# Kernel optimization log

Measured on AMD Instinct MI355X. Metric: run time of the kernel, lower is better.

## Reference

```python
import jax, jax.numpy as jnp
import numpy as np

MARGIN = 0.2  # contrastive margin
# sim_type_dot = 'MISA': max over image regions, mean over (valid) words


def setup_inputs() -> dict:
    key = jax.random.key(0)
    k1, k2, k3, k4 = jax.random.split(key, 4)
    B, R, W, D = 128, 36, 60, 1024
    im = jax.random.normal(k1, (B, R, D), dtype=jnp.float32)
    s = jax.random.normal(k2, (B, W, D), dtype=jnp.float32)
    x = jax.random.normal(k3, (B, W, D), dtype=jnp.float32)  # unused in math, kept for API fidelity
    s_l = jax.random.randint(k4, (B,), 1, W + 1)  # caption lengths in [1, W]
    return {"im": im, "s": s, "s_l": s_l, "x": x}


def _scores(im, s, s_l):
    # im: (B, R, D) images; s: (B, W, D) captions; s_l: (B,) lengths
    B, W = s.shape[0], s.shape[1]
    # matchmap M[i, j, r, w] = <image j region r, caption i word w>
    M = jnp.einsum('jrd,iwd->ijrw', im, s)
    # MISA: max over regions r, then mean over the n_word valid words of caption i
    M_max = M.max(axis=2)                                   # (i, j, w)
    word_mask = (jnp.arange(W)[None, :] < s_l[:, None]).astype(M.dtype)  # (i, w)
    sims = (M_max * word_mask[:, None, :]).sum(axis=-1) / s_l[:, None].astype(M.dtype)  # (i, j)
    # original layout: scores[image j, caption i]
    return sims.T


def reference(im, s, s_l, x):
    scores = _scores(im, s, s_l)                 # (B, B)
    diag = jnp.diagonal(scores)[:, None]         # (B, 1)
    cost_s = jnp.maximum(MARGIN + scores - diag, 0.0)
    cost_im = jnp.maximum(MARGIN + scores - diag.T, 0.0)
    eye = jnp.eye(scores.shape[0], dtype=bool)
    cost_s = jnp.where(eye, 0.0, cost_s)
    cost_im = jnp.where(eye, 0.0, cost_im)
    return cost_s.sum() + cost_im.sum()
```

## Files before the change

### kernel.cpp

```cpp
#include <hip/hip_runtime.h>
#include <hip/hip_bf16.h>
#include <stdint.h>

#define B_SZ 128
#define R_SZ 36
#define RP_SZ 48
#define W_SZ 60
#define WP_SZ 64
#define D_SZ 1024
#define MARGIN 0.2f

#define ATILE_B (192 * 64)
#define BTILE_B (256 * 64)

typedef __attribute__((ext_vector_type(4))) float f32x4;
typedef __attribute__((ext_vector_type(2))) long longx2;

typedef __attribute__((address_space(3))) unsigned int lds_u32;
typedef const __attribute__((address_space(1))) unsigned int glb_u32;

__device__ __forceinline__ void gload16(const unsigned char* g, unsigned char* l) {
    __builtin_amdgcn_global_load_lds((glb_u32*)g, (lds_u32*)l, 16, 0, 0);
}

__global__ __launch_bounds__(256) void convert_fp8_kernel(
        const float* __restrict__ im, const float* __restrict__ s,
        unsigned char* __restrict__ imb, unsigned char* __restrict__ sb) {
    const int nA = B_SZ * RP_SZ * 64;
    const int nB = B_SZ * WP_SZ * 64;
    int i = blockIdx.x * 256 + threadIdx.x;
    const float* srcrow;
    unsigned char* dst;
    int gran, row;
    if (i < nA) {
        gran = i & 63; row = i >> 6;
        int j = row / RP_SZ, r = row % RP_SZ;
        int rs = r < R_SZ ? r : R_SZ - 1;
        srcrow = im + ((size_t)(j * R_SZ + rs) << 10);
        dst = imb + (size_t)i * 16;
    } else {
        int i2 = i - nA;
        if (i2 >= nB) return;
        gran = i2 & 63; row = i2 >> 6;
        int j = row >> 6, w = row & 63;
        int ws = w < W_SZ ? w : W_SZ - 1;
        srcrow = s + ((size_t)(j * W_SZ + ws) << 10);
        dst = sb + (size_t)i2 * 16;
    }
    const int kb = gran >> 2, g = gran & 3;
    uint4 o;
    unsigned int* op = (unsigned int*)&o;
#pragma unroll
    for (int q = 0; q < 4; ++q) {
        const int kq = kb * 64 + (q >> 1) * 32 + g * 8 + (q & 1) * 4;
        float4 v = *reinterpret_cast<const float4*>(srcrow + kq);
        int w32 = __builtin_amdgcn_cvt_pk_fp8_f32(v.x, v.y, 0, false);
        w32 = __builtin_amdgcn_cvt_pk_fp8_f32(v.z, v.w, w32, true);
        op[q] = (unsigned int)w32;
    }
    *reinterpret_cast<uint4*>(dst) = o;
}

__global__ __launch_bounds__(512, 2) void scores_kernel(
        const unsigned char* __restrict__ imb,
        const unsigned char* __restrict__ sb,
        const int* __restrict__ s_l,
        float* __restrict__ S)
{
    __shared__ __align__(16) unsigned char As[2 * ATILE_B];
    __shared__ __align__(16) unsigned char Bs[2 * BTILE_B];

    const int tid  = threadIdx.x;
    const int wid  = tid >> 6;
    const int lane = tid & 63;
    const int l15  = lane & 15;
    const int kgrp = lane >> 4;
    const int wr   = wid >> 2;
    const int wc   = wid & 3;

    int bid = blockIdx.x;
    int k8  = bid & 7;
    int w   = bid >> 3;
    int jtg = w >> 5;
    int sw  = w & 31;
    int it  = k8 * 4 + (sw >> 3);
    int jt  = jtg * 8 + (sw & 7);

    const int drow = lane >> 2;
    const int sgr  = ((lane & 3) ^ ((lane >> 3) & 3)) * 16;

    const unsigned char* gsrc[4];
    unsigned char* gdst0[4];
    int tsz[4];
#pragma unroll
    for (int si = 0; si < 4; ++si) {
        int c = wid + si * 8;
        if (c < 12) {
            gsrc[si]  = imb + (size_t)(jt * 192 + c * 16 + drow) * 1024 + sgr;
            gdst0[si] = As + c * 1024 + lane * 16;
            tsz[si]   = ATILE_B;
        } else if (c < 28) {
            int b = c - 12;
            gsrc[si]  = sb + (size_t)(it * 256 + b * 16 + drow) * 1024 + sgr;
            gdst0[si] = Bs + b * 1024 + lane * 16;
            tsz[si]   = BTILE_B;
        }
    }

    const int slot0 = (kgrp ^ ((l15 >> 1) & 3)) * 16;
    int abase[6];
#pragma unroll
    for (int rf = 0; rf < 6; ++rf)
        abase[rf] = (wr * 96 + rf * 16 + l15) * 64 + slot0;
    int bbase[4];
#pragma unroll
    for (int cf = 0; cf < 4; ++cf)
        bbase[cf] = (wc * 64 + cf * 16 + l15) * 64 + slot0;

    f32x4 acc[6][4] = {};

#pragma unroll
    for (int si = 0; si < 4; ++si) {
        int c = wid + si * 8;
        if (c < 28) gload16(gsrc[si], gdst0[si]);
    }
    asm volatile("s_waitcnt vmcnt(0)" ::: "memory");
    __builtin_amdgcn_s_barrier();

#pragma unroll 2
    for (int kt = 0; kt < 16; ++kt) {
        const int cur = kt & 1;
        const unsigned char* Ac = As + cur * ATILE_B;
        const unsigned char* Bc = Bs + cur * BTILE_B;

        if (kt < 15) {
            const int ko = (kt + 1) * 64;
            const int nb = cur ^ 1;
#pragma unroll
            for (int si = 0; si < 4; ++si) {
                int c = wid + si * 8;
                if (c < 28) gload16(gsrc[si] + ko, gdst0[si] + nb * tsz[si]);
            }
        }

        longx2 afr[6], bfr[4];
#pragma unroll
        for (int rf = 0; rf < 6; ++rf)
            afr[rf] = *reinterpret_cast<const longx2*>(Ac + abase[rf]);
#pragma unroll
        for (int cf = 0; cf < 4; ++cf)
            bfr[cf] = *reinterpret_cast<const longx2*>(Bc + bbase[cf]);

        __builtin_amdgcn_s_setprio(1);
#pragma unroll
        for (int k2 = 0; k2 < 2; ++k2)
#pragma unroll
            for (int rf = 0; rf < 6; ++rf)
#pragma unroll
                for (int cf = 0; cf < 4; ++cf)
                    acc[rf][cf] = __builtin_amdgcn_mfma_f32_16x16x32_fp8_fp8(
                        afr[rf][k2], bfr[cf][k2], acc[rf][cf], 0, 0, 0);
        __builtin_amdgcn_s_setprio(0);

        if (kt < 15) {
            asm volatile("s_waitcnt vmcnt(0)" ::: "memory");
            __builtin_amdgcn_s_barrier();
        }
    }

    const int i_cap = it * 4 + wc;
    const int nw = s_l[i_cap];
    const float inv = 1.0f / (float)nw;
#pragma unroll
    for (int h = 0; h < 2; ++h) {
        float sum = 0.0f;
#pragma unroll
        for (int cf = 0; cf < 4; ++cf) {
            float m = acc[h * 3][cf][0];
#pragma unroll
            for (int rf = h * 3; rf < h * 3 + 3; ++rf)
#pragma unroll
                for (int e = 0; e < 4; ++e)
                    m = fmaxf(m, acc[rf][cf][e]);
            m = fmaxf(m, __shfl_xor(m, 16));
            m = fmaxf(m, __shfl_xor(m, 32));
            int wv = cf * 16 + l15;
            if (wv < nw) sum += m;
        }
        sum += __shfl_xor(sum, 1);
        sum += __shfl_xor(sum, 2);
        sum += __shfl_xor(sum, 4);
        sum += __shfl_xor(sum, 8);
        if (lane == 0) {
            int j_img = jt * 4 + wr * 2 + h;
            S[j_img * B_SZ + i_cap] = sum * inv;
        }
    }
}

__global__ __launch_bounds__(1024) void loss_kernel(
        const float* __restrict__ S, float* __restrict__ out) {
    __shared__ float diag[B_SZ];
    __shared__ float red[1024];
    int t = threadIdx.x;
    if (t < B_SZ) diag[t] = S[t * (B_SZ + 1)];
    __syncthreads();
    float acc = 0.0f;
    for (int idx = t; idx < B_SZ * B_SZ; idx += 1024) {
        int a = idx >> 7, b = idx & (B_SZ - 1);
        if (a != b) {
            float v = S[idx];
            acc += fmaxf(MARGIN + v - diag[a], 0.0f)
                 + fmaxf(MARGIN + v - diag[b], 0.0f);
        }
    }
    red[t] = acc;
    __syncthreads();
    for (int s = 512; s > 0; s >>= 1) {
        if (t < s) red[t] += red[t + s];
        __syncthreads();
    }
    if (t == 0) out[0] = red[0];
}

extern "C" void kernel_launch(void* const* d_in, const int* in_sizes, int n_in,
                              void* d_out, int out_size, void* d_ws, size_t ws_size,
                              hipStream_t stream) {
    const float* im  = (const float*)d_in[0];
    const float* s   = (const float*)d_in[1];
    const int*   s_l = (const int*)d_in[2];

    const int n_im_pad = B_SZ * RP_SZ * D_SZ;
    const int n_s_pad  = B_SZ * WP_SZ * D_SZ;

    unsigned char* imb = (unsigned char*)d_ws;
    unsigned char* sb  = imb + n_im_pad;
    float* S = (float*)(sb + n_s_pad);

    const int ngran = (n_im_pad + n_s_pad) / 16;
    convert_fp8_kernel<<<(ngran + 255) / 256, 256, 0, stream>>>(im, s, imb, sb);

    scores_kernel<<<1024, 512, 0, stream>>>(imb, sb, s_l, S);

    loss_kernel<<<1, 1024, 0, stream>>>(S, (float*)d_out);
}
```

Measured before the change: 89.97 us.

## Drop region padding and pack image tiles densely with per-lane group max

Image regions are no longer padded from 36 to 48 rows. Each block now loads a 144-row tile holding four images back to back, and the eight waves tile only the caption columns, each covering all 144 rows × 32 words. This removes the MFMA work and load traffic that went to padding rows. In exchange, the epilogue must split the max by image when a 16-row fragment straddles an image boundary, and the two halves of each caption's words are combined through LDS with an extra block barrier. Launch bounds now request 4 blocks per CU, which limits registers per thread and could cause spills.

Measured after the change: 75.21 us, median of 3. 16.4% less time.

```diff
diff --git a/kernel.cpp b/kernel.cpp
--- a/kernel.cpp
+++ b/kernel.cpp
@@ -4,14 +4,14 @@
 
 #define B_SZ 128
 #define R_SZ 36
-#define RP_SZ 48
 #define W_SZ 60
 #define WP_SZ 64
 #define D_SZ 1024
 #define MARGIN 0.2f
 
-#define ATILE_B (192 * 64)
+#define ATILE_B (144 * 64)
 #define BTILE_B (256 * 64)
+#define BUFB    (ATILE_B + BTILE_B)
 
 typedef __attribute__((ext_vector_type(4))) float f32x4;
 typedef __attribute__((ext_vector_type(2))) long longx2;
@@ -26,22 +26,22 @@
 __global__ __launch_bounds__(256) void convert_fp8_kernel(
         const float* __restrict__ im, const float* __restrict__ s,
         unsigned char* __restrict__ imb, unsigned char* __restrict__ sb) {
-    const int nA = B_SZ * RP_SZ * 64;
+    const int nA = B_SZ * R_SZ * 64;
     const int nB = B_SZ * WP_SZ * 64;
     int i = blockIdx.x * 256 + threadIdx.x;
     const float* srcrow;
     unsigned char* dst;
-    int gran, row;
+    int gran;
     if (i < nA) {
-        gran = i & 63; row = i >> 6;
-        int j = row / RP_SZ, r = row % RP_SZ;
-        int rs = r < R_SZ ? r : R_SZ - 1;
-        srcrow = im + ((size_t)(j * R_SZ + rs) << 10);
+        gran = i & 63;
+        int row = i >> 6;
+        srcrow = im + ((size_t)row << 10);
         dst = imb + (size_t)i * 16;
     } else {
         int i2 = i - nA;
         if (i2 >= nB) return;
-        gran = i2 & 63; row = i2 >> 6;
+        gran = i2 & 63;
+        int row = i2 >> 6;
         int j = row >> 6, w = row & 63;
         int ws = w < W_SZ ? w : W_SZ - 1;
         srcrow = s + ((size_t)(j * W_SZ + ws) << 10);
@@ -61,22 +61,20 @@
     *reinterpret_cast<uint4*>(dst) = o;
 }
 
-__global__ __launch_bounds__(512, 2) void scores_kernel(
+__global__ __launch_bounds__(512, 4) void scores_kernel(
         const unsigned char* __restrict__ imb,
-        const unsigned char* __restrict__ sb,
+        const unsigned char* __restrict__ sbp,
         const int* __restrict__ s_l,
         float* __restrict__ S)
 {
-    __shared__ __align__(16) unsigned char As[2 * ATILE_B];
-    __shared__ __align__(16) unsigned char Bs[2 * BTILE_B];
+    __shared__ __align__(16) unsigned char LDS[2 * BUFB];
+    __shared__ float red2[8][4];
 
     const int tid  = threadIdx.x;
-    const int wid  = tid >> 6;
+    const int wc   = tid >> 6;
     const int lane = tid & 63;
     const int l15  = lane & 15;
     const int kgrp = lane >> 4;
-    const int wr   = wid >> 2;
-    const int wc   = wid & 3;
 
     int bid = blockIdx.x;
     int k8  = bid & 7;
@@ -90,39 +88,33 @@
     const int sgr  = ((lane & 3) ^ ((lane >> 3) & 3)) * 16;
 
     const unsigned char* gsrc[4];
-    unsigned char* gdst0[4];
-    int tsz[4];
+    int ldso[4];
 #pragma unroll
     for (int si = 0; si < 4; ++si) {
-        int c = wid + si * 8;
-        if (c < 12) {
-            gsrc[si]  = imb + (size_t)(jt * 192 + c * 16 + drow) * 1024 + sgr;
-            gdst0[si] = As + c * 1024 + lane * 16;
-            tsz[si]   = ATILE_B;
-        } else if (c < 28) {
-            int b = c - 12;
-            gsrc[si]  = sb + (size_t)(it * 256 + b * 16 + drow) * 1024 + sgr;
-            gdst0[si] = Bs + b * 1024 + lane * 16;
-            tsz[si]   = BTILE_B;
+        int c = wc + si * 8;
+        if (c < 9) {
+            gsrc[si] = imb + (size_t)(jt * 144 + c * 16 + drow) * 1024 + sgr;
+            ldso[si] = c * 1024 + lane * 16;
+        } else if (c < 25) {
+            int b = c - 9;
+            gsrc[si] = sbp + (size_t)(it * 256 + b * 16 + drow) * 1024 + sgr;
+            ldso[si] = ATILE_B + b * 1024 + lane * 16;
         }
     }
 
     const int slot0 = (kgrp ^ ((l15 >> 1) & 3)) * 16;
-    int abase[6];
-#pragma unroll
-    for (int rf = 0; rf < 6; ++rf)
-        abase[rf] = (wr * 96 + rf * 16 + l15) * 64 + slot0;
-    int bbase[4];
-#pragma unroll
-    for (int cf = 0; cf < 4; ++cf)
-        bbase[cf] = (wc * 64 + cf * 16 + l15) * 64 + slot0;
-
-    f32x4 acc[6][4] = {};
+    const int abase = l15 * 64 + slot0;
+    int bbase[2];
+#pragma unroll
+    for (int cf = 0; cf < 2; ++cf)
+        bbase[cf] = ATILE_B + (wc * 32 + cf * 16 + l15) * 64 + slot0;
+
+    f32x4 acc[9][2] = {};
 
 #pragma unroll
     for (int si = 0; si < 4; ++si) {
-        int c = wid + si * 8;
-        if (c < 28) gload16(gsrc[si], gdst0[si]);
+        int c = wc + si * 8;
+        if (c < 25) gload16(gsrc[si], LDS + ldso[si]);
     }
     asm volatile("s_waitcnt vmcnt(0)" ::: "memory");
     __builtin_amdgcn_s_barrier();
@@ -130,36 +122,34 @@
 #pragma unroll 2
     for (int kt = 0; kt < 16; ++kt) {
         const int cur = kt & 1;
-        const unsigned char* Ac = As + cur * ATILE_B;
-        const unsigned char* Bc = Bs + cur * BTILE_B;
+        const unsigned char* base = LDS + cur * BUFB;
+
+        longx2 bfr[2];
+#pragma unroll
+        for (int cf = 0; cf < 2; ++cf)
+            bfr[cf] = *reinterpret_cast<const longx2*>(base + bbase[cf]);
 
         if (kt < 15) {
             const int ko = (kt + 1) * 64;
-            const int nb = cur ^ 1;
+            unsigned char* dstb = LDS + (cur ^ 1) * BUFB;
 #pragma unroll
             for (int si = 0; si < 4; ++si) {
-                int c = wid + si * 8;
-                if (c < 28) gload16(gsrc[si] + ko, gdst0[si] + nb * tsz[si]);
+                int c = wc + si * 8;
+                if (c < 25) gload16(gsrc[si] + ko, dstb + ldso[si]);
             }
         }
 
-        longx2 afr[6], bfr[4];
-#pragma unroll
-        for (int rf = 0; rf < 6; ++rf)
-            afr[rf] = *reinterpret_cast<const longx2*>(Ac + abase[rf]);
-#pragma unroll
-        for (int cf = 0; cf < 4; ++cf)
-            bfr[cf] = *reinterpret_cast<const longx2*>(Bc + bbase[cf]);
-
         __builtin_amdgcn_s_setprio(1);
 #pragma unroll
-        for (int k2 = 0; k2 < 2; ++k2)
-#pragma unroll
-            for (int rf = 0; rf < 6; ++rf)
-#pragma unroll
-                for (int cf = 0; cf < 4; ++cf)
+        for (int rf = 0; rf < 9; ++rf) {
+            longx2 af = *reinterpret_cast<const longx2*>(base + abase + rf * 1024);
+#pragma unroll
+            for (int k2 = 0; k2 < 2; ++k2)
+#pragma unroll
+                for (int cf = 0; cf < 2; ++cf)
                     acc[rf][cf] = __builtin_amdgcn_mfma_f32_16x16x32_fp8_fp8(
-                        afr[rf][k2], bfr[cf][k2], acc[rf][cf], 0, 0, 0);
+                        af[k2], bfr[cf][k2], acc[rf][cf], 0, 0, 0);
+        }
         __builtin_amdgcn_s_setprio(0);
 
         if (kt < 15) {
@@ -168,32 +158,62 @@
         }
     }
 
-    const int i_cap = it * 4 + wc;
+    float mm[2][4];
+#pragma unroll
+    for (int cf = 0; cf < 2; ++cf)
+#pragma unroll
+        for (int g = 0; g < 4; ++g) mm[cf][g] = -3.4e38f;
+
+#pragma unroll
+    for (int cf = 0; cf < 2; ++cf)
+#pragma unroll
+        for (int rf = 0; rf < 9; ++rf)
+#pragma unroll
+            for (int e = 0; e < 4; ++e) {
+                const int row0 = rf * 16 + e;
+                const int g0 = row0 / 36;
+                const int g1 = (row0 + 12) / 36;
+                float v = acc[rf][cf][e];
+                if (g0 == g1) {
+                    mm[cf][g0] = fmaxf(mm[cf][g0], v);
+                } else {
+                    int lr = row0 + 4 * kgrp;
+                    if (lr >= g1 * 36) mm[cf][g1] = fmaxf(mm[cf][g1], v);
+                    else               mm[cf][g0] = fmaxf(mm[cf][g0], v);
+                }
+            }
+
+    const int i_cap = it * 4 + (wc >> 1);
     const int nw = s_l[i_cap];
-    const float inv = 1.0f / (float)nw;
-#pragma unroll
-    for (int h = 0; h < 2; ++h) {
-        float sum = 0.0f;
-#pragma unroll
-        for (int cf = 0; cf < 4; ++cf) {
-            float m = acc[h * 3][cf][0];
-#pragma unroll
-            for (int rf = h * 3; rf < h * 3 + 3; ++rf)
-#pragma unroll
-                for (int e = 0; e < 4; ++e)
-                    m = fmaxf(m, acc[rf][cf][e]);
+    float sums[4];
+#pragma unroll
+    for (int g = 0; g < 4; ++g) {
+        float sg = 0.0f;
+#pragma unroll
+        for (int cf = 0; cf < 2; ++cf) {
+            float m = mm[cf][g];
             m = fmaxf(m, __shfl_xor(m, 16));
             m = fmaxf(m, __shfl_xor(m, 32));
-            int wv = cf * 16 + l15;
-            if (wv < nw) sum += m;
-        }
-        sum += __shfl_xor(sum, 1);
-        sum += __shfl_xor(sum, 2);
-        sum += __shfl_xor(sum, 4);
-        sum += __shfl_xor(sum, 8);
-        if (lane == 0) {
-            int j_img = jt * 4 + wr * 2 + h;
-            S[j_img * B_SZ + i_cap] = sum * inv;
+            int wv = (wc & 1) * 32 + cf * 16 + l15;
+            if (wv < nw) sg += m;
+        }
+        sg += __shfl_xor(sg, 1);
+        sg += __shfl_xor(sg, 2);
+        sg += __shfl_xor(sg, 4);
+        sg += __shfl_xor(sg, 8);
+        sums[g] = sg;
+    }
+    if (lane == 0) {
+#pragma unroll
+        for (int g = 0; g < 4; ++g) red2[wc][g] = sums[g];
+    }
+    __syncthreads();
+    if ((wc & 1) == 0 && lane == 0) {
+        const float inv = 1.0f / (float)nw;
+#pragma unroll
+        for (int g = 0; g < 4; ++g) {
+            int j_img = jt * 4 + g;
+            S[j_img * B_SZ + i_cap] = (red2[wc][g] + red2[wc + 1][g]) * inv;
         }
     }
 }
@@ -230,14 +250,14 @@
     const float* s   = (const float*)d_in[1];
     const int*   s_l = (const int*)d_in[2];
 
-    const int n_im_pad = B_SZ * RP_SZ * D_SZ;
-    const int n_s_pad  = B_SZ * WP_SZ * D_SZ;
+    const int n_im = B_SZ * R_SZ * D_SZ;
+    const int n_s  = B_SZ * WP_SZ * D_SZ;
 
     unsigned char* imb = (unsigned char*)d_ws;
-    unsigned char* sb  = imb + n_im_pad;
-    float* S = (float*)(sb + n_s_pad);
-
-    const int ngran = (n_im_pad + n_s_pad) / 16;
+    unsigned char* sb  = imb + n_im;
+    float* S = (float*)(sb + n_s);
+
+    const int ngran = (n_im + n_s) / 16;
     convert_fp8_kernel<<<(ngran + 255) / 256, 256, 0, stream>>>(im, s, imb, sb);
 
     scores_kernel<<<1024, 512, 0, stream>>>(imb, sb, s_l, S);
```
